# Kernel optimization log

Measured on AMD Instinct MI355X. Metric: run time of the kernel, lower is better.

Reference implementation:

```python
import jax, jax.numpy as jnp
import numpy as np

VOCAB, EMB, HID, T, B, NCLS = 50000, 300, 512, 128, 256, 3


def _lstm_final_h(x, lens, W, b):
    """TF BasicLSTMCell semantics (gate order i,j,f,o; forget_bias=1.0) with
    dynamic_rnn sequence_length masking; returns final hidden state [B, HID].
    x: [B, T, EMB] float, lens: [B] int, W: [EMB+HID, 4*HID], b: [4*HID].
    """
    xt = jnp.swapaxes(x, 0, 1)                       # [T, B, EMB]
    mask = jnp.arange(T)[:, None] < lens[None, :]    # [T, B]

    def step(carry, inp):
        c, h = carry
        x_t, m = inp
        z = jnp.concatenate([x_t, h], axis=-1) @ W + b   # [B, 4*HID]
        i, j, f, o = jnp.split(z, 4, axis=-1)
        c_new = c * jax.nn.sigmoid(f + 1.0) + jax.nn.sigmoid(i) * jnp.tanh(j)
        h_new = jnp.tanh(c_new) * jax.nn.sigmoid(o)
        m = m[:, None]
        return (jnp.where(m, c_new, c), jnp.where(m, h_new, h)), None

    init = (jnp.zeros((x.shape[0], HID), x.dtype),
            jnp.zeros((x.shape[0], HID), x.dtype))
    (c, h), _ = jax.lax.scan(step, init, (xt, mask))
    return h


def setup_inputs() -> dict:
    key = jax.random.key(0)
    ks = jax.random.split(key, 12)
    s = 0.05
    return {
        "left_ids": jax.random.randint(ks[0], (B, T), 0, VOCAB, dtype=jnp.int32),
        "right_ids": jax.random.randint(ks[1], (B, T), 0, VOCAB, dtype=jnp.int32),
        "left_len": jax.random.randint(ks[2], (B,), 1, T + 1, dtype=jnp.int32),
        "right_len": jax.random.randint(ks[3], (B,), 1, T + 1, dtype=jnp.int32),
        "embeddings": jax.random.normal(ks[4], (VOCAB, EMB), jnp.float32) * s,
        "W_l": jax.random.normal(ks[5], (EMB + HID, 4 * HID), jnp.float32) * s,
        "b_l": jnp.zeros((4 * HID,), jnp.float32),
        "W_r": jax.random.normal(ks[6], (EMB + HID, 4 * HID), jnp.float32) * s,
        "b_r": jnp.zeros((4 * HID,), jnp.float32),
        "W_d": jax.random.normal(ks[7], (2 * HID, NCLS), jnp.float32) * s,
        "b_d": jnp.zeros((NCLS,), jnp.float32),
    }


def reference(left_ids, right_ids, left_len, right_len,
              embeddings, W_l, b_l, W_r, b_r, W_d, b_d):
    left_x = embeddings[left_ids]      # [B, T, EMB]
    right_x = embeddings[right_ids]    # [B, T, EMB]
    h_l = _lstm_final_h(left_x, left_len, W_l, b_l)     # [B, HID]
    h_r = _lstm_final_h(right_x, right_len, W_r, b_r)   # [B, HID]
    logits = jnp.concatenate([h_l, h_r], axis=1) @ W_d + b_d  # [B, NCLS]
    return logits
```

## Files before the change

### kernel.cpp

```cpp
#include <hip/hip_runtime.h>


using bf16x8 = __attribute__((ext_vector_type(8))) __bf16;
using f32x4  = __attribute__((ext_vector_type(4))) float;
using u32x4  = __attribute__((ext_vector_type(4))) unsigned int;
typedef unsigned short u16;
typedef unsigned int u32;
typedef unsigned long long u64;

#define NT 128
#define ROWB 1664
#define SWZ(row, off) ((off) ^ (((row) & 7) << 4))

#define LGKM0  asm volatile("s_waitcnt lgkmcnt(0)" ::: "memory")
#define VM0    asm volatile("s_waitcnt vmcnt(0)" ::: "memory")
#define BAR()  __builtin_amdgcn_s_barrier()
#define SCHED0 __builtin_amdgcn_sched_barrier(0)

__device__ __forceinline__ u16 f2bf(float f) {
  union { float f; unsigned u; } v; v.f = f;
  unsigned r = v.u + 0x7fffu + ((v.u >> 16) & 1u);
  return (u16)(r >> 16);
}
__device__ __forceinline__ float sigf(float x) { return 1.f / (1.f + __expf(-x)); }
__device__ __forceinline__ float tanhf_(float x) { return 2.f / (1.f + __expf(-2.f * x)) - 1.f; }

__device__ __forceinline__ void setA26(bf16x8 (&A)[26], int kt, bf16x8 v) {
  switch (kt) {
    case 0:A[0]=v;break;  case 1:A[1]=v;break;  case 2:A[2]=v;break;
    case 3:A[3]=v;break;  case 4:A[4]=v;break;  case 5:A[5]=v;break;
    case 6:A[6]=v;break;  case 7:A[7]=v;break;  case 8:A[8]=v;break;
    case 9:A[9]=v;break;  case 10:A[10]=v;break; case 11:A[11]=v;break;
    case 12:A[12]=v;break; case 13:A[13]=v;break; case 14:A[14]=v;break;
    case 15:A[15]=v;break; case 16:A[16]=v;break; case 17:A[17]=v;break;
    case 18:A[18]=v;break; case 19:A[19]=v;break; case 20:A[20]=v;break;
    case 21:A[21]=v;break; case 22:A[22]=v;break; case 23:A[23]=v;break;
    case 24:A[24]=v;break; case 25:A[25]=v;break;
  }
}

__global__ __launch_bounds__(256, 1) void lstm_persist(
    const int* __restrict__ lids, const int* __restrict__ rids,
    const int* __restrict__ llen, const int* __restrict__ rlen,
    const float* __restrict__ emb,
    const float* __restrict__ Wl, const float* __restrict__ bl,
    const float* __restrict__ Wr, const float* __restrict__ br,
    u64* __restrict__ hbuf,
    float* __restrict__ hfin,
    u32* __restrict__ flags)
{
  __shared__ __align__(16) unsigned char sB[32 * ROWB];
  __shared__ __align__(8)  u16 sH[32][36];
  __shared__ int sI[4096];

  const int tid = threadIdx.x;
  const int w = tid >> 6, l = tid & 63;
  const int bid = blockIdx.x;
  const int xcd = bid & 7, idx = bid >> 3;
  const int grp = xcd * 2 + (idx >> 4);
  const int ct  = idx & 15;
  const int lstm = grp >> 3, bt = grp & 7;
  const int b0 = bt * 32, u0 = ct * 32;

  const int*   ids  = lstm ? rids : lids;
  const int*   lenp = lstm ? rlen : llen;
  const float* W    = lstm ? Wr : Wl;
  const float* bv   = lstm ? br : bl;

  bf16x8 A0[26], A1[26];
  {
    float* sW = (float*)sB;
    for (int kc = 0; kc < 13; ++kc) {
      for (int i = 0; i < 32; ++i) {
        int id2 = tid + i * 256;
        int c = id2 & 31, r = (id2 >> 5) & 63, g = id2 >> 11;
        int kk = kc * 64 + r;
        float v = 0.f;
        if (kk < 300)       v = W[kk * 2048 + g * 512 + u0 + c];
        else if (kk >= 320) v = W[(kk - 20) * 2048 + g * 512 + u0 + c];
        sW[(g * 64 + r) * 32 + c] = v;
      }
      __syncthreads();
      #pragma unroll
      for (int kt2 = 0; kt2 < 2; ++kt2) {
        int kt = kc * 2 + kt2;
        #pragma unroll
        for (int mf2 = 0; mf2 < 2; ++mf2) {
          int mf = w * 2 + mf2;
          int rho = mf * 16 + (l & 15);
          int du = rho >> 2, g = rho & 3;
          union { u16 s[8]; bf16x8 v; } tmp;
          #pragma unroll
          for (int j = 0; j < 8; ++j) {
            int kr = kt2 * 32 + ((l >> 4) << 3) + j;
            tmp.s[j] = f2bf(sW[(g * 64 + kr) * 32 + du]);
          }
          if (mf2 == 0) setA26(A0, kt, tmp.v); else setA26(A1, kt, tmp.v);
        }
      }
      __syncthreads();
    }
  }

  if (tid < 160) {
    int row = tid / 5, c5 = tid - (tid / 5) * 5;
    *(u64*)(sB + row * ROWB + SWZ(row, 600 + c5 * 8)) = 0ULL;
  }
  {
    const int* src = ids + b0 * NT;
    #pragma unroll
    for (int i = 0; i < 4; ++i)
      *(int4*)&sI[(tid + i * 256) * 4] = *(const int4*)&src[(tid + i * 256) * 4];
  }

  int ldsoff[10], sirow[10], foff[10];
  #pragma unroll
  for (int i = 0; i < 10; ++i) {
    int id2 = tid + i * 256;
    int row = (id2 < 2400) ? id2 / 75 : 0;
    int f4 = id2 - row * 75;
    ldsoff[i] = row * ROWB + SWZ(row, f4 * 8);
    sirow[i]  = row * NT;
    foff[i]   = f4 * 4;
  }
  int hoff[16];
  #pragma unroll
  for (int i = 0; i < 16; ++i) {
    int id2 = tid + i * 256;
    int row = id2 >> 7, c8 = id2 & 127;
    hoff[i] = row * ROWB + SWZ(row, 640 + c8 * 8);
  }

  int lenn[2];
  lenn[0] = lenp[b0 + (l & 15)];
  lenn[1] = lenp[b0 + 16 + (l & 15)];
  float bia[2][4];
  #pragma unroll
  for (int mf2 = 0; mf2 < 2; ++mf2) {
    int du = w * 8 + mf2 * 4 + (l >> 4);
    #pragma unroll
    for (int g = 0; g < 4; ++g) bia[mf2][g] = bv[g * 512 + u0 + du];
  }
  float cst[2][2] = {{0.f, 0.f}, {0.f, 0.f}};
  float hst[2][2] = {{0.f, 0.f}, {0.f, 0.f}};
  __syncthreads();

  float4 px[10];
  #pragma unroll
  for (int i = 0; i < 10; ++i)
    if (i < 9 || tid < 96) {
      int eid = sI[sirow[i]];
      float4 xv = *(const float4*)(emb + eid * 300 + foff[i]);
      u64 pk = (u64)f2bf(xv.x) | ((u64)f2bf(xv.y) << 16) |
               ((u64)f2bf(xv.z) << 32) | ((u64)f2bf(xv.w) << 48);
      *(u64*)(sB + ldsoff[i]) = pk;
    }
  #pragma unroll
  for (int i = 0; i < 10; ++i)
    if (i < 9 || tid < 96) {
      int eid = sI[sirow[i] + 1];
      px[i] = *(const float4*)(emb + eid * 300 + foff[i]);
    }
  __syncthreads();

  const int r0 = l & 15, r1 = 16 + (l & 15);

  f32x4 xacc[2][2];
  xacc[0][0] = {0.f,0.f,0.f,0.f}; xacc[0][1] = {0.f,0.f,0.f,0.f};
  xacc[1][0] = {0.f,0.f,0.f,0.f}; xacc[1][1] = {0.f,0.f,0.f,0.f};
  #pragma unroll
  for (int kt = 0; kt < 10; ++kt) {
    int kb = kt * 64 + ((l >> 4) << 4);
    bf16x8 B0 = __builtin_bit_cast(bf16x8, *(const u32x4*)(sB + r0 * ROWB + SWZ(r0, kb)));
    bf16x8 B1 = __builtin_bit_cast(bf16x8, *(const u32x4*)(sB + r1 * ROWB + SWZ(r1, kb)));
    xacc[0][0] = __builtin_amdgcn_mfma_f32_16x16x32_bf16(A0[kt], B0, xacc[0][0], 0, 0, 0);
    xacc[0][1] = __builtin_amdgcn_mfma_f32_16x16x32_bf16(A0[kt], B1, xacc[0][1], 0, 0, 0);
    xacc[1][0] = __builtin_amdgcn_mfma_f32_16x16x32_bf16(A1[kt], B0, xacc[1][0], 0, 0, 0);
    xacc[1][1] = __builtin_amdgcn_mfma_f32_16x16x32_bf16(A1[kt], B1, xacc[1][1], 0, 0, 0);
  }

  for (int t = 0; t < NT; ++t) {
    if (t > 0) {
      {
        const u32* fl = flags + (grp * 2 + ((t & 1) ^ 1)) * 16;
        u32 fv; bool ok;
        do {
          fv = __hip_atomic_load(&fl[l & 15], __ATOMIC_RELAXED,
                                 __HIP_MEMORY_SCOPE_AGENT);
          ok = __all(fv >= (u32)t);
          if (!ok) __builtin_amdgcn_s_sleep(1);
        } while (!ok);
      }
      SCHED0;
      const u64* hsrc = hbuf + (((lstm * 2 + ((t & 1) ^ 1)) * 256) + b0) * 128;
      u64 hld[16];
      #pragma unroll
      for (int i = 0; i < 16; ++i)
        hld[i] = __hip_atomic_load(&hsrc[tid + i * 256], __ATOMIC_RELAXED,
                                   __HIP_MEMORY_SCOPE_AGENT);
      #pragma unroll
      for (int i = 0; i < 16; ++i) *(u64*)(sB + hoff[i]) = hld[i];
      LGKM0; BAR(); SCHED0;
      #pragma unroll
      for (int kt = 10; kt < 26; ++kt) {
        int kb = kt * 64 + ((l >> 4) << 4);
        bf16x8 B0 = __builtin_bit_cast(bf16x8, *(const u32x4*)(sB + r0 * ROWB + SWZ(r0, kb)));
        bf16x8 B1 = __builtin_bit_cast(bf16x8, *(const u32x4*)(sB + r1 * ROWB + SWZ(r1, kb)));
        xacc[0][0] = __builtin_amdgcn_mfma_f32_16x16x32_bf16(A0[kt], B0, xacc[0][0], 0, 0, 0);
        xacc[0][1] = __builtin_amdgcn_mfma_f32_16x16x32_bf16(A0[kt], B1, xacc[0][1], 0, 0, 0);
        xacc[1][0] = __builtin_amdgcn_mfma_f32_16x16x32_bf16(A1[kt], B0, xacc[1][0], 0, 0, 0);
        xacc[1][1] = __builtin_amdgcn_mfma_f32_16x16x32_bf16(A1[kt], B1, xacc[1][1], 0, 0, 0);
      }
    }

    #pragma unroll
    for (int mf2 = 0; mf2 < 2; ++mf2)
      #pragma unroll
      for (int n = 0; n < 2; ++n) {
        f32x4 z = xacc[mf2][n];
        float zi = z[0] + bia[mf2][0];
        float zj = z[1] + bia[mf2][1];
        float zf = z[2] + bia[mf2][2];
        float zo = z[3] + bia[mf2][3];
        float cn = cst[mf2][n] * sigf(zf + 1.f) + sigf(zi) * tanhf_(zj);
        float hn = tanhf_(cn) * sigf(zo);
        if (t < lenn[n]) { cst[mf2][n] = cn; hst[mf2][n] = hn; }
        sH[n * 16 + (l & 15)][w * 8 + mf2 * 4 + (l >> 4)] = f2bf(hst[mf2][n]);
      }
    LGKM0; BAR(); SCHED0;

    {
      int bbL = tid >> 3, u8 = tid & 7;
      u64 pk = *(const u64*)&sH[bbL][u8 * 4];
      u64* hdst = hbuf + (((lstm * 2 + (t & 1)) * 256) + b0 + bbL) * 128 + (u0 >> 2) + u8;
      __hip_atomic_store(hdst, pk, __ATOMIC_RELAXED, __HIP_MEMORY_SCOPE_AGENT);
    }
    #pragma unroll
    for (int i = 0; i < 10; ++i)
      if (i < 9 || tid < 96) {
        float4 xv = px[i];
        u64 pk = (u64)f2bf(xv.x) | ((u64)f2bf(xv.y) << 16) |
                 ((u64)f2bf(xv.z) << 32) | ((u64)f2bf(xv.w) << 48);
        *(u64*)(sB + ldsoff[i]) = pk;
      }
    VM0; LGKM0; BAR();

    if (tid == 0)
      __hip_atomic_store(&flags[(grp * 2 + (t & 1)) * 16 + ct], (u32)(t + 1),
                         __ATOMIC_RELAXED, __HIP_MEMORY_SCOPE_AGENT);
    SCHED0;

    {
      int tn2 = (t + 2) & (NT - 1);
      #pragma unroll
      for (int i = 0; i < 10; ++i)
        if (i < 9 || tid < 96) {
          int eid = sI[sirow[i] + tn2];
          px[i] = *(const float4*)(emb + eid * 300 + foff[i]);
        }
    }
    xacc[0][0] = {0.f,0.f,0.f,0.f}; xacc[0][1] = {0.f,0.f,0.f,0.f};
    xacc[1][0] = {0.f,0.f,0.f,0.f}; xacc[1][1] = {0.f,0.f,0.f,0.f};
    #pragma unroll
    for (int kt = 0; kt < 10; ++kt) {
      int kb = kt * 64 + ((l >> 4) << 4);
      bf16x8 B0 = __builtin_bit_cast(bf16x8, *(const u32x4*)(sB + r0 * ROWB + SWZ(r0, kb)));
      bf16x8 B1 = __builtin_bit_cast(bf16x8, *(const u32x4*)(sB + r1 * ROWB + SWZ(r1, kb)));
      xacc[0][0] = __builtin_amdgcn_mfma_f32_16x16x32_bf16(A0[kt], B0, xacc[0][0], 0, 0, 0);
      xacc[0][1] = __builtin_amdgcn_mfma_f32_16x16x32_bf16(A0[kt], B1, xacc[0][1], 0, 0, 0);
      xacc[1][0] = __builtin_amdgcn_mfma_f32_16x16x32_bf16(A1[kt], B0, xacc[1][0], 0, 0, 0);
      xacc[1][1] = __builtin_amdgcn_mfma_f32_16x16x32_bf16(A1[kt], B1, xacc[1][1], 0, 0, 0);
    }
  }

  #pragma unroll
  for (int mf2 = 0; mf2 < 2; ++mf2)
    #pragma unroll
    for (int n = 0; n < 2; ++n) {
      int bb = b0 + n * 16 + (l & 15);
      int uu = u0 + w * 8 + mf2 * 4 + (l >> 4);
      hfin[lstm * (256 * 512) + bb * 512 + uu] = hst[mf2][n];
    }
}

__global__ void dense_out(const float* __restrict__ hfin,
                          const float* __restrict__ Wd, const float* __restrict__ bd,
                          float* __restrict__ out) {
  const int b = blockIdx.x, l = threadIdx.x;
  float a0 = 0.f, a1 = 0.f, a2 = 0.f;
  for (int i = l; i < 1024; i += 64) {
    float hv = (i < 512) ? hfin[b * 512 + i] : hfin[256 * 512 + b * 512 + (i - 512)];
    a0 += hv * Wd[i * 3 + 0];
    a1 += hv * Wd[i * 3 + 1];
    a2 += hv * Wd[i * 3 + 2];
  }
  #pragma unroll
  for (int off = 32; off > 0; off >>= 1) {
    a0 += __shfl_down(a0, off);
    a1 += __shfl_down(a1, off);
    a2 += __shfl_down(a2, off);
  }
  if (l == 0) {
    out[b * 3 + 0] = a0 + bd[0];
    out[b * 3 + 1] = a1 + bd[1];
    out[b * 3 + 2] = a2 + bd[2];
  }
}

extern "C" void kernel_launch(void* const* d_in, const int* in_sizes, int n_in,
                              void* d_out, int out_size, void* d_ws, size_t ws_size,
                              hipStream_t stream) {
  const int*   lids = (const int*)d_in[0];
  const int*   rids = (const int*)d_in[1];
  const int*   llen = (const int*)d_in[2];
  const int*   rlen = (const int*)d_in[3];
  const float* emb  = (const float*)d_in[4];
  const float* Wl   = (const float*)d_in[5];
  const float* bl   = (const float*)d_in[6];
  const float* Wr   = (const float*)d_in[7];
  const float* br   = (const float*)d_in[8];
  const float* Wd   = (const float*)d_in[9];
  const float* bd   = (const float*)d_in[10];

  unsigned char* ws = (unsigned char*)d_ws;
  u32*   flags = (u32*)ws;
  u64*   hbuf  = (u64*)(ws + 4096);
  float* hfin  = (float*)(ws + 4096 + (1u << 20));

  hipMemsetAsync(flags, 0, 2048, stream);
  hipLaunchKernelGGL(lstm_persist, dim3(256), dim3(256), 0, stream,
                     lids, rids, llen, rlen, emb, Wl, bl, Wr, br, hbuf, hfin, flags);
  hipLaunchKernelGGL(dense_out, dim3(256), dim3(64), 0, stream,
                     hfin, Wd, bd, (float*)d_out);
}
```

Measured before the change: 659.6 us.

## Use per-wave flags, speculative flag prefetch, and packed bf16 conversion

Each wave now publishes its own completion flag once its own h stores have drained, so the block barrier before signalling is gone and no thread waits on the whole block. A speculative load of the 64 per-wave flags is issued after the input-projection MFMAs, so the next step's spin often finds them already satisfied without another round trip. The fp32-to-bf16 packing switches to the hardware v_cvt_pk_bf16_f32 instruction. In exchange the flag array grows to 64 entries per group and the workspace offsets and memset size grow with it. The wave-level memory ordering (store, vmcnt wait, flag) needs care to stay correct.

```diff
diff --git a/kernel.cpp b/kernel.cpp
--- a/kernel.cpp
+++ b/kernel.cpp
@@ -21,6 +21,14 @@
   union { float f; unsigned u; } v; v.f = f;
   unsigned r = v.u + 0x7fffu + ((v.u >> 16) & 1u);
   return (u16)(r >> 16);
+}
+__device__ __forceinline__ u32 cvtpk(float lo, float hi) {
+  u32 r;
+  asm("v_cvt_pk_bf16_f32 %0, %1, %2" : "=v"(r) : "v"(lo), "v"(hi));
+  return r;
+}
+__device__ __forceinline__ u64 pack4(float4 xv) {
+  return (u64)cvtpk(xv.x, xv.y) | ((u64)cvtpk(xv.z, xv.w) << 32);
 }
 __device__ __forceinline__ float sigf(float x) { return 1.f / (1.f + __expf(-x)); }
 __device__ __forceinline__ float tanhf_(float x) { return 2.f / (1.f + __expf(-2.f * x)) - 1.f; }
@@ -151,9 +159,7 @@
     if (i < 9 || tid < 96) {
       int eid = sI[sirow[i]];
       float4 xv = *(const float4*)(emb + eid * 300 + foff[i]);
-      u64 pk = (u64)f2bf(xv.x) | ((u64)f2bf(xv.y) << 16) |
-               ((u64)f2bf(xv.z) << 32) | ((u64)f2bf(xv.w) << 48);
-      *(u64*)(sB + ldsoff[i]) = pk;
+      *(u64*)(sB + ldsoff[i]) = pack4(xv);
     }
   #pragma unroll
   for (int i = 0; i < 10; ++i)
@@ -179,17 +185,18 @@
     xacc[1][1] = __builtin_amdgcn_mfma_f32_16x16x32_bf16(A1[kt], B1, xacc[1][1], 0, 0, 0);
   }
 
+  u32 fa = 0;
+
   for (int t = 0; t < NT; ++t) {
     if (t > 0) {
       {
-        const u32* fl = flags + (grp * 2 + ((t & 1) ^ 1)) * 16;
-        u32 fv; bool ok;
-        do {
-          fv = __hip_atomic_load(&fl[l & 15], __ATOMIC_RELAXED,
-                                 __HIP_MEMORY_SCOPE_AGENT);
-          ok = __all(fv >= (u32)t);
+        const u32* fl = flags + (grp * 2 + ((t & 1) ^ 1)) * 64;
+        bool ok = __all(fa >= (u32)t);
+        while (!ok) {
+          fa = __hip_atomic_load(&fl[l], __ATOMIC_RELAXED, __HIP_MEMORY_SCOPE_AGENT);
+          ok = __all(fa >= (u32)t);
           if (!ok) __builtin_amdgcn_s_sleep(1);
-        } while (!ok);
+        }
       }
       SCHED0;
       const u64* hsrc = hbuf + (((lstm * 2 + ((t & 1) ^ 1)) * 256) + b0) * 128;
@@ -237,18 +244,14 @@
     }
     #pragma unroll
     for (int i = 0; i < 10; ++i)
-      if (i < 9 || tid < 96) {
-        float4 xv = px[i];
-        u64 pk = (u64)f2bf(xv.x) | ((u64)f2bf(xv.y) << 16) |
-                 ((u64)f2bf(xv.z) << 32) | ((u64)f2bf(xv.w) << 48);
-        *(u64*)(sB + ldsoff[i]) = pk;
-      }
-    VM0; LGKM0; BAR();
-
-    if (tid == 0)
-      __hip_atomic_store(&flags[(grp * 2 + (t & 1)) * 16 + ct], (u32)(t + 1),
+      if (i < 9 || tid < 96)
+        *(u64*)(sB + ldsoff[i]) = pack4(px[i]);
+    VM0;
+
+    if (l == 0)
+      __hip_atomic_store(&flags[(grp * 2 + (t & 1)) * 64 + ct * 4 + w], (u32)(t + 1),
                          __ATOMIC_RELAXED, __HIP_MEMORY_SCOPE_AGENT);
-    SCHED0;
+    LGKM0; BAR(); SCHED0;
 
     {
       int tn2 = (t + 2) & (NT - 1);
@@ -271,6 +274,9 @@
       xacc[1][0] = __builtin_amdgcn_mfma_f32_16x16x32_bf16(A1[kt], B0, xacc[1][0], 0, 0, 0);
       xacc[1][1] = __builtin_amdgcn_mfma_f32_16x16x32_bf16(A1[kt], B1, xacc[1][1], 0, 0, 0);
     }
+
+    fa = __hip_atomic_load(&flags[(grp * 2 + (t & 1)) * 64 + l],
+                           __ATOMIC_RELAXED, __HIP_MEMORY_SCOPE_AGENT);
   }
 
   #pragma unroll
@@ -324,10 +330,10 @@
 
   unsigned char* ws = (unsigned char*)d_ws;
   u32*   flags = (u32*)ws;
-  u64*   hbuf  = (u64*)(ws + 4096);
-  float* hfin  = (float*)(ws + 4096 + (1u << 20));
-
-  hipMemsetAsync(flags, 0, 2048, stream);
+  u64*   hbuf  = (u64*)(ws + 8192);
+  float* hfin  = (float*)(ws + 8192 + (1u << 20));
+
+  hipMemsetAsync(flags, 0, 8192, stream);
   hipLaunchKernelGGL(lstm_persist, dim3(256), dim3(256), 0, stream,
                      lids, rids, llen, rlen, emb, Wl, bl, Wr, br, hbuf, hfin, flags);
   hipLaunchKernelGGL(dense_out, dim3(256), dim3(64), 0, stream,
```

Result: no change. 652.6 us (-1.1%).
